# Performance work log

Hardware: AMD Instinct MI355X
Metric: run time of the kernel (lower is better)

The kernel has to match this reference:

```python
import jax, jax.numpy as jnp
import numpy as np
from jax import lax

T = 36          # number of frames (dictionary rows)
MAXITER = 100   # fista maxIter
LAMBD0 = 0.01   # base sparsity weight (scaled by 1/L as in torch code)
TOL = 1e-4      # convergence tolerance


def build_dictionary(Drr, Dtheta, n_frames):
    # Vectorized version of the Python loop over i in range(T).
    i = jnp.arange(n_frames, dtype=Drr.dtype)                     # (T,)
    powr = Drr[None, :] ** i[:, None]                             # (T,N)  Drr^i (Drr>0)
    sign = jnp.where(i[:, None] % 2 == 0, 1.0, -1.0).astype(Drr.dtype)  # (-Drr)^i = (-1)^i Drr^i
    ang = i[:, None] * Dtheta[None, :]
    cosm, sinm = jnp.cos(ang), jnp.sin(ang)
    ones = jnp.ones((n_frames, 1), Drr.dtype)
    dic = jnp.concatenate(
        [ones, powr * cosm, sign * powr * cosm, powr * sinm, sign * powr * sinm],
        axis=1)                                                   # (T, 4N+1)
    G = jnp.linalg.norm(dic, axis=0)                              # column norms
    G = jnp.where(G == 0, jnp.sqrt(jnp.asarray(n_frames, Drr.dtype)), G)
    return dic / G


def softshrink(z, lambd):
    return jnp.sign(z) * jnp.maximum(jnp.abs(z) - lambd, 0.0)


def fista(D, Y):
    # D: (T,K), Y: (B,T,P). torch broadcasts the 2D init state; we carry full (B,K,P).
    DtD = D.T @ D                                                 # (K,K)
    L = jnp.linalg.norm(DtD)      # torch.norm(DtD, 2) = flattened 2-norm (Frobenius)
    linv = 1.0 / L
    DtY = jnp.einsum('tk,btp->bkp', D, Y) * linv                  # (B,K,P)
    K = DtD.shape[0]
    A = jnp.eye(K, dtype=D.dtype) - DtD * linv                    # (K,K)
    lambd = LAMBD0 * linv
    x0 = jnp.zeros_like(DtY)

    def cond(c):
        ii, t, x, y, Ay, done = c
        return (ii < MAXITER) & jnp.logical_not(done)

    def body(c):
        ii, t, x, y, Ay_prev, done = c
        Ay = jnp.einsum('kj,bjp->bkp', A, y)                      # (B,K,P)
        x_new = softshrink(Ay + DtY, lambd)
        t_new = (1.0 + jnp.sqrt(1.0 + 4.0 * t * t)) / 2.0
        tt = (t - 1.0) / t_new
        y_new = (1.0 + tt) * x_new - tt * x
        done = (jnp.linalg.norm((x - x_new).ravel()) / K) < TOL   # device-side convergence test
        return (ii + 1, t_new, x_new, y_new, Ay, done)

    init = (jnp.asarray(0, jnp.int32), jnp.asarray(1.0, D.dtype), x0, x0, x0,
            jnp.asarray(False))
    ii, t, x, y, Ay, done = lax.while_loop(cond, body, init)
    return x, Ay


def setup_inputs() -> dict:
    key = jax.random.key(0)
    k1, k2, k3 = jax.random.split(key, 3)
    N, B, P = 40, 4, 16384
    Drr = (0.8 + 0.2 * jax.random.uniform(k1, (N,))).astype(jnp.float32)   # pole radii near 1
    Dtheta = (np.pi * jax.random.uniform(k2, (N,))).astype(jnp.float32)    # pole angles
    x = jax.random.normal(k3, (B, T, P), dtype=jnp.float32)
    return {"x": x, "Drr": Drr, "Dtheta": Dtheta}


def reference(x, Drr, Dtheta):
    D = build_dictionary(Drr, Dtheta, T)
    sparsecode, _ = fista(D, x)
    return sparsecode
```

## Files before the change

kernel.cpp:

```cpp
#include <hip/hip_runtime.h>
#include <hip/hip_bf16.h>

typedef __attribute__((ext_vector_type(8))) short bf16x8;
typedef __attribute__((ext_vector_type(4))) float f32x4;

#define NITER 100
#define MT 2
#define WS_D     0
#define WS_SCAL  5904
#define WS_A     8192
#define WS_FLOATS (8192 + 192*200)

__device__ __forceinline__ unsigned short f2bf(float x) {
  unsigned u = __builtin_bit_cast(unsigned, x);
  u += 0x7fffu + ((u >> 16) & 1u);
  return (unsigned short)(u >> 16);
}
__device__ __forceinline__ float bf2f(unsigned short h) {
  unsigned u = ((unsigned)h) << 16;
  return __builtin_bit_cast(float, u);
}
__device__ __forceinline__ float ubit(unsigned u) { return __builtin_bit_cast(float, u); }
__device__ __forceinline__ unsigned cvt_pk_bf16(float a, float b) {
  unsigned r;
  asm("v_cvt_pk_bf16_f32 %0, %1, %2" : "=v"(r) : "v"(a), "v"(b));
  return r;
}

__global__ __launch_bounds__(256) void prep_kernel(const float* __restrict__ Drr,
                                                   const float* __restrict__ Dth,
                                                   float* __restrict__ ws)
{
  __shared__ float sD[36 * 164];
  __shared__ float sIG[164];
  __shared__ float sRed[256];
  const int tid = (int)threadIdx.x;

  for (int idx = tid; idx < 36 * 164; idx += 256) {
    int t = idx / 164, k = idx - t * 164;
    float v = 0.0f;
    if (k == 0) v = 1.0f;
    else if (k < 161) {
      int km = k - 1, g = km / 40, n = km - g * 40;
      float pw  = powf(Drr[n], (float)t);
      float ang = (float)t * Dth[n];
      float base = ((g & 2) == 0) ? cosf(ang) : sinf(ang);
      v = pw * base;
      if ((g & 1) && (t & 1)) v = -v;
    }
    sD[idx] = v;
  }
  __syncthreads();
  if (tid < 161) {
    float s = 0.0f;
    for (int t = 0; t < 36; ++t) { float d = sD[t * 164 + tid]; s += d * d; }
    float g = sqrtf(s);
    if (g == 0.0f) g = 6.0f;
    sIG[tid] = 1.0f / g;
  }
  __syncthreads();
  for (int idx = tid; idx < 36 * 164; idx += 256) {
    int k = idx % 164;
    if (k < 161) sD[idx] *= sIG[k];
  }
  __syncthreads();
  {
    float local = 0.0f;
    for (int idx = tid; idx < 36 * 36; idx += 256) {
      int t = idx / 36, t2 = idx - t * 36;
      float dot = 0.0f;
      for (int k = 0; k < 161; ++k) dot += sD[t * 164 + k] * sD[t2 * 164 + k];
      local += dot * dot;
    }
    sRed[tid] = local;
  }
  __syncthreads();
  for (int off = 128; off > 0; off >>= 1) {
    if (tid < off) sRed[tid] += sRed[tid + off];
    __syncthreads();
  }
  const float linv = 1.0f / sqrtf(sRed[0]);

  if (blockIdx.x == 0) {
    for (int idx = tid; idx < 36 * 164; idx += 256) ws[WS_D + idx] = sD[idx];
    if (tid == 0) { ws[WS_SCAL] = linv; ws[WS_SCAL + 1] = 0.01f * linv; }
  }
  const int ENT = (192 * 200 + (int)gridDim.x - 1) / (int)gridDim.x;
  const int base = (int)blockIdx.x * ENT;
  for (int i = tid; i < ENT; i += 256) {
    int e = base + i;
    if (e >= 192 * 200) break;
    int r = e / 200, j = e - r * 200;
    float a = 0.0f;
    if (r < 161 && j < 161) {
      float dot = 0.0f;
      for (int t = 0; t < 36; ++t) dot += sD[t * 164 + r] * sD[t * 164 + j];
      a = ((r == j) ? 1.0f : 0.0f) - dot * linv;
    }
    ws[WS_A + e] = a;
  }
}

union SmemU {
  struct {
    float sD[36 * 164];
    float sIG[164];
    float sRed[512];
  } su;
  unsigned char bounce[2][16 * 384];
};

template <int USE_WS>
__global__ __launch_bounds__(512, 2) void fista_kernel(
    const float* __restrict__ X, const float* __restrict__ Drr,
    const float* __restrict__ Dth, float* __restrict__ out,
    const float* __restrict__ ws)
{
  __shared__ SmemU sm;
  float* sD = sm.su.sD;

  const int tid  = (int)threadIdx.x;
  const int lane = tid & 63;
  const int wv   = tid >> 6;
  const int cl   = lane & 15;
  const int hi   = lane >> 4;
  const int t0   = (wv < 3) ? wv * 2 : 3 + wv;
  const int ntl  = (wv < 3) ? 2 : 1;

  float linv, lambd;
  if constexpr (USE_WS) {
    for (int idx = tid; idx < 36 * 164; idx += 512) sD[idx] = ws[WS_D + idx];
    linv  = ws[WS_SCAL];
    lambd = ws[WS_SCAL + 1];
    __syncthreads();
  } else {
    for (int idx = tid; idx < 36 * 164; idx += 512) {
      int t = idx / 164, k = idx - t * 164;
      float v = 0.0f;
      if (k == 0) v = 1.0f;
      else if (k < 161) {
        int km = k - 1, g = km / 40, n = km - g * 40;
        float pw  = powf(Drr[n], (float)t);
        float ang = (float)t * Dth[n];
        float base = ((g & 2) == 0) ? cosf(ang) : sinf(ang);
        v = pw * base;
        if ((g & 1) && (t & 1)) v = -v;
      }
      sD[idx] = v;
    }
    __syncthreads();
    if (tid < 161) {
      float s = 0.0f;
      for (int t = 0; t < 36; ++t) { float d = sD[t * 164 + tid]; s += d * d; }
      float g = sqrtf(s);
      if (g == 0.0f) g = 6.0f;
      sm.su.sIG[tid] = 1.0f / g;
    }
    __syncthreads();
    for (int idx = tid; idx < 36 * 164; idx += 512) {
      int k = idx % 164;
      if (k < 161) sD[idx] *= sm.su.sIG[k];
    }
    __syncthreads();
    {
      float local = 0.0f;
      for (int idx = tid; idx < 36 * 36; idx += 512) {
        int t = idx / 36, t2 = idx - t * 36;
        float dot = 0.0f;
        for (int k = 0; k < 161; ++k) dot += sD[t * 164 + k] * sD[t2 * 164 + k];
        local += dot * dot;
      }
      sm.su.sRed[tid] = local;
    }
    __syncthreads();
    for (int off = 256; off > 0; off >>= 1) {
      if (tid < off) sm.su.sRed[tid] += sm.su.sRed[tid + off];
      __syncthreads();
    }
    linv  = 1.0f / sqrtf(sm.su.sRed[0]);
    lambd = 0.01f * linv;
  }

  bf16x8 Ah[MT][6], Al[MT][6];
  #pragma unroll
  for (int tau = 0; tau < MT; ++tau) if (tau < ntl) {
    const int r = (t0 + tau) * 16 + cl;
    #pragma unroll
    for (int kt = 0; kt < 6; ++kt) {
      const int k0 = kt * 32 + hi * 8;
      float av[8];
      if constexpr (USE_WS) {
        const float* ap = ws + WS_A + r * 200 + k0;
        f32x4 a0 = *reinterpret_cast<const f32x4*>(ap);
        f32x4 a1 = *reinterpret_cast<const f32x4*>(ap + 4);
        av[0]=a0[0]; av[1]=a0[1]; av[2]=a0[2]; av[3]=a0[3];
        av[4]=a1[0]; av[5]=a1[1]; av[6]=a1[2]; av[7]=a1[3];
      } else {
        float acc8[8];
        #pragma unroll
        for (int j = 0; j < 8; ++j) acc8[j] = 0.0f;
        if (r < 161) {
          for (int t = 0; t < 36; ++t) {
            float vr = sD[t * 164 + r];
            #pragma unroll
            for (int j = 0; j < 8; ++j) acc8[j] += vr * sD[t * 164 + k0 + j];
          }
        }
        #pragma unroll
        for (int j = 0; j < 8; ++j) {
          int k = k0 + j;
          float a = 0.0f;
          if (r < 161 && k < 161) {
            a = -acc8[j] * linv;
            if (r == k) a += 1.0f;
          }
          av[j] = a;
        }
      }
      bf16x8 vh, vl;
      #pragma unroll
      for (int j = 0; j < 8; ++j) {
        unsigned short h = f2bf(av[j]);
        vh[j] = (short)h;
        vl[j] = (short)f2bf(av[j] - bf2f(h));
      }
      Ah[tau][kt] = vh;
      Al[tau][kt] = vl;
    }
  }

  const int c = (int)blockIdx.x * 16 + cl;
  const int b = c >> 14;
  const int p = c & 16383;
  const float* Xc = X + (size_t)b * (36 * 16384) + p;

  f32x4 P0[MT], P1[MT], xe[MT];
  #pragma unroll
  for (int tau = 0; tau < MT; ++tau)
    #pragma unroll
    for (int q = 0; q < 4; ++q) { P0[tau][q] = 0.0f; P1[tau][q] = 0.0f; xe[tau][q] = 0.0f; }

  for (int t = 0; t < 36; ++t) {
    float yv = Xc[(size_t)t * 16384];
    #pragma unroll
    for (int tau = 0; tau < MT; ++tau) if (tau < ntl) {
      const int rt = t0 + tau;
      f32x4 df = *reinterpret_cast<const f32x4*>(sD + t * 164 + rt * 16 + hi * 4);
      #pragma unroll
      for (int q = 0; q < 4; ++q) P0[tau][q] += df[q] * yv;
    }
  }
  #pragma unroll
  for (int tau = 0; tau < MT; ++tau)
    #pragma unroll
    for (int q = 0; q < 4; ++q) {
      int r = (t0 + tau) * 16 + hi * 4 + q;
      P0[tau][q] = (r < 161) ? P0[tau][q] * linv : 0.0f;
    }
  __syncthreads();

  for (int i = tid; i < 2 * 16 * 384 / 16; i += 512) {
    f32x4 z = {0.0f, 0.0f, 0.0f, 0.0f};
    reinterpret_cast<f32x4*>(sm.bounce[0])[i] = z;
  }
  __syncthreads();

  unsigned char* colb = sm.bounce[0] + cl * 384;
  const unsigned swz = (unsigned)((cl & 7) << 4);
  unsigned char* rdA[6];
  #pragma unroll
  for (int kt = 0; kt < 6; ++kt)
    rdA[kt] = colb + (((unsigned)(kt * 64 + hi * 16)) ^ swz);
  unsigned char* wrA[MT];
  #pragma unroll
  for (int tau = 0; tau < MT; ++tau)
    wrA[tau] = colb + (((unsigned)((t0 + tau) * 32 + hi * 8)) ^ swz);

  float tcur = 1.0f, tt = 0.0f;

  auto step = [&](f32x4 (&PC)[MT], f32x4 (&PN)[MT], int boff) {
    const float ttp = tt, c1 = 1.0f + ttp;
    #pragma unroll
    for (int tau = 0; tau < MT; ++tau) if (tau < ntl) {
      float dq_[4];
      #pragma unroll
      for (int q = 0; q < 4; ++q) {
        float u  = c1 * PC[tau][q] - ttp * PN[tau][q];
        float aa = fmaxf(fabsf(u) - lambd, 0.0f);
        float xn = __builtin_copysignf(aa, u);
        dq_[q] = xn - xe[tau][q];
      }
      unsigned w0 = cvt_pk_bf16(dq_[0], dq_[1]);
      unsigned w1 = cvt_pk_bf16(dq_[2], dq_[3]);
      xe[tau][0] += ubit(w0 << 16);
      xe[tau][1] += ubit(w0 & 0xffff0000u);
      xe[tau][2] += ubit(w1 << 16);
      xe[tau][3] += ubit(w1 & 0xffff0000u);
      *reinterpret_cast<uint2*>(wrA[tau] + boff) = make_uint2(w0, w1);
    }
    __syncthreads();
    bf16x8 bh[6];
    #pragma unroll
    for (int kt = 0; kt < 6; ++kt)
      bh[kt] = *reinterpret_cast<const bf16x8*>(rdA[kt] + boff);
    #pragma unroll
    for (int kt = 0; kt < 6; ++kt) {
      #pragma unroll
      for (int tau = 0; tau < MT; ++tau) if (tau < ntl) {
        f32x4 acc = (kt == 0) ? PC[tau] : PN[tau];
        acc = __builtin_amdgcn_mfma_f32_16x16x32_bf16(Ah[tau][kt], bh[kt], acc, 0, 0, 0);
        acc = __builtin_amdgcn_mfma_f32_16x16x32_bf16(Al[tau][kt], bh[kt], acc, 0, 0, 0);
        PN[tau] = acc;
      }
    }
    float tn = 0.5f * (1.0f + sqrtf(1.0f + 4.0f * tcur * tcur));
    tt = (tcur - 1.0f) / tn;
    tcur = tn;
  };

  #pragma unroll 1
  for (int it = 0; it < NITER / 2; ++it) {
    step(P0, P1, 0);
    step(P1, P0, 16 * 384);
  }

  float* op = out + (size_t)b * (161 * 16384) + p;
  #pragma unroll
  for (int tau = 0; tau < MT; ++tau) if (tau < ntl) {
    #pragma unroll
    for (int q = 0; q < 4; ++q) {
      int r = (t0 + tau) * 16 + hi * 4 + q;
      if (r < 161) op[(size_t)r * 16384] = xe[tau][q];
    }
  }
}

extern "C" void kernel_launch(void* const* d_in, const int* in_sizes, int n_in,
                              void* d_out, int out_size, void* d_ws, size_t ws_size,
                              hipStream_t stream) {
  const float* X   = (const float*)d_in[0];
  const float* Drr = (const float*)d_in[1];
  const float* Dth = (const float*)d_in[2];
  float* out = (float*)d_out;
  (void)in_sizes; (void)n_in; (void)out_size;

  if (ws_size >= (size_t)WS_FLOATS * sizeof(float)) {
    float* ws = (float*)d_ws;
    prep_kernel<<<dim3(64), dim3(256), 0, stream>>>(Drr, Dth, ws);
    fista_kernel<1><<<dim3(4096), dim3(512), 0, stream>>>(X, Drr, Dth, out, ws);
  } else {
    fista_kernel<0><<<dim3(4096), dim3(512), 0, stream>>>(X, Drr, Dth, out, nullptr);
  }
}
```

Measured before the change: 1.320 ms.

## Interleave two column groups per block to overlap MFMA with shrink step

Each block now handles two independent 16-column groups, with 6 waves that each own two row tiles. The shrink/update of one group is interleaved with the MFMA matvec of the other through double-buffered LDS bounce buffers, so barrier latency and dependency stalls can be hidden. The FISTA momentum coefficients are precomputed once into LDS instead of being recomputed with sqrt/div every step. A is stored pre-split into bf16 hi/lo in the workspace. The cost is more registers per thread for the duplicated accumulators and more LDS per block, which may reduce occupancy.

```diff
diff --git a/kernel.cpp b/kernel.cpp
--- a/kernel.cpp
+++ b/kernel.cpp
@@ -5,11 +5,10 @@
 typedef __attribute__((ext_vector_type(4))) float f32x4;
 
 #define NITER 100
-#define MT 2
-#define WS_D     0
 #define WS_SCAL  5904
-#define WS_A     8192
-#define WS_FLOATS (8192 + 192*200)
+#define WS_AH    8192
+#define WS_FLOATS (8192 + 19200 + 19200)
+#define BUF1 12288
 
 __device__ __forceinline__ unsigned short f2bf(float x) {
   unsigned u = __builtin_bit_cast(unsigned, x);
@@ -82,9 +81,11 @@
   const float linv = 1.0f / sqrtf(sRed[0]);
 
   if (blockIdx.x == 0) {
-    for (int idx = tid; idx < 36 * 164; idx += 256) ws[WS_D + idx] = sD[idx];
+    for (int idx = tid; idx < 36 * 164; idx += 256) ws[idx] = sD[idx];
     if (tid == 0) { ws[WS_SCAL] = linv; ws[WS_SCAL + 1] = 0.01f * linv; }
   }
+  unsigned short* AH16 = reinterpret_cast<unsigned short*>(ws + WS_AH);
+  unsigned short* AL16 = AH16 + 192 * 200;
   const int ENT = (192 * 200 + (int)gridDim.x - 1) / (int)gridDim.x;
   const int base = (int)blockIdx.x * ENT;
   for (int i = tid; i < ENT; i += 256) {
@@ -97,44 +98,38 @@
       for (int t = 0; t < 36; ++t) dot += sD[t * 164 + r] * sD[t * 164 + j];
       a = ((r == j) ? 1.0f : 0.0f) - dot * linv;
     }
-    ws[WS_A + e] = a;
-  }
-}
-
-union SmemU {
-  struct {
-    float sD[36 * 164];
-    float sIG[164];
-    float sRed[512];
-  } su;
-  unsigned char bounce[2][16 * 384];
-};
+    unsigned short ah = f2bf(a);
+    AH16[e] = ah;
+    AL16[e] = f2bf(a - bf2f(ah));
+  }
+}
 
 template <int USE_WS>
-__global__ __launch_bounds__(512, 2) void fista_kernel(
+__global__ __launch_bounds__(384, 2) void fista_kernel(
     const float* __restrict__ X, const float* __restrict__ Drr,
     const float* __restrict__ Dth, float* __restrict__ out,
     const float* __restrict__ ws)
 {
-  __shared__ SmemU sm;
+  __shared__ union {
+    struct { float sD[36 * 164]; float sIG[164]; float sRed[512]; } su;
+    unsigned char bounce[2][2][16 * 384];
+  } sm;
+  __shared__ float2 sTT[NITER];
+
   float* sD = sm.su.sD;
-
   const int tid  = (int)threadIdx.x;
   const int lane = tid & 63;
   const int wv   = tid >> 6;
   const int cl   = lane & 15;
   const int hi   = lane >> 4;
-  const int t0   = (wv < 3) ? wv * 2 : 3 + wv;
-  const int ntl  = (wv < 3) ? 2 : 1;
 
   float linv, lambd;
   if constexpr (USE_WS) {
-    for (int idx = tid; idx < 36 * 164; idx += 512) sD[idx] = ws[WS_D + idx];
+    for (int idx = tid; idx < 36 * 164; idx += 384) sD[idx] = ws[idx];
     linv  = ws[WS_SCAL];
     lambd = ws[WS_SCAL + 1];
-    __syncthreads();
   } else {
-    for (int idx = tid; idx < 36 * 164; idx += 512) {
+    for (int idx = tid; idx < 36 * 164; idx += 384) {
       int t = idx / 164, k = idx - t * 164;
       float v = 0.0f;
       if (k == 0) v = 1.0f;
@@ -157,20 +152,21 @@
       sm.su.sIG[tid] = 1.0f / g;
     }
     __syncthreads();
-    for (int idx = tid; idx < 36 * 164; idx += 512) {
+    for (int idx = tid; idx < 36 * 164; idx += 384) {
       int k = idx % 164;
       if (k < 161) sD[idx] *= sm.su.sIG[k];
     }
     __syncthreads();
     {
       float local = 0.0f;
-      for (int idx = tid; idx < 36 * 36; idx += 512) {
+      for (int idx = tid; idx < 36 * 36; idx += 384) {
         int t = idx / 36, t2 = idx - t * 36;
         float dot = 0.0f;
         for (int k = 0; k < 161; ++k) dot += sD[t * 164 + k] * sD[t2 * 164 + k];
         local += dot * dot;
       }
       sm.su.sRed[tid] = local;
+      if (tid < 128) sm.su.sRed[384 + tid] = 0.0f;
     }
     __syncthreads();
     for (int off = 256; off > 0; off >>= 1) {
@@ -181,21 +177,36 @@
     lambd = 0.01f * linv;
   }
 
-  bf16x8 Ah[MT][6], Al[MT][6];
-  #pragma unroll
-  for (int tau = 0; tau < MT; ++tau) if (tau < ntl) {
-    const int r = (t0 + tau) * 16 + cl;
-    #pragma unroll
-    for (int kt = 0; kt < 6; ++kt) {
-      const int k0 = kt * 32 + hi * 8;
-      float av[8];
-      if constexpr (USE_WS) {
-        const float* ap = ws + WS_A + r * 200 + k0;
-        f32x4 a0 = *reinterpret_cast<const f32x4*>(ap);
-        f32x4 a1 = *reinterpret_cast<const f32x4*>(ap + 4);
-        av[0]=a0[0]; av[1]=a0[1]; av[2]=a0[2]; av[3]=a0[3];
-        av[4]=a1[0]; av[5]=a1[1]; av[6]=a1[2]; av[7]=a1[3];
-      } else {
+  if (tid == 0) {
+    float t = 1.0f;
+    for (int k = 0; k < NITER; ++k) {
+      float tn = 0.5f * (1.0f + sqrtf(1.0f + 4.0f * t * t));
+      float tt = (t - 1.0f) / tn;
+      sTT[k] = make_float2(tt, 1.0f + tt);
+      t = tn;
+    }
+  }
+
+  bf16x8 Ah[2][6], Al[2][6];
+  if constexpr (USE_WS) {
+    const unsigned short* AH16 = reinterpret_cast<const unsigned short*>(ws + WS_AH);
+    const unsigned short* AL16 = AH16 + 192 * 200;
+    #pragma unroll
+    for (int tau = 0; tau < 2; ++tau) {
+      const int r = (2 * wv + tau) * 16 + cl;
+      #pragma unroll
+      for (int kt = 0; kt < 6; ++kt) {
+        Ah[tau][kt] = *reinterpret_cast<const bf16x8*>(AH16 + r * 200 + kt * 32 + hi * 8);
+        Al[tau][kt] = *reinterpret_cast<const bf16x8*>(AL16 + r * 200 + kt * 32 + hi * 8);
+      }
+    }
+  } else {
+    #pragma unroll
+    for (int tau = 0; tau < 2; ++tau) {
+      const int r = (2 * wv + tau) * 16 + cl;
+      #pragma unroll
+      for (int kt = 0; kt < 6; ++kt) {
+        const int k0 = kt * 32 + hi * 8;
         float acc8[8];
         #pragma unroll
         for (int j = 0; j < 8; ++j) acc8[j] = 0.0f;
@@ -206,6 +217,7 @@
             for (int j = 0; j < 8; ++j) acc8[j] += vr * sD[t * 164 + k0 + j];
           }
         }
+        bf16x8 vh, vl;
         #pragma unroll
         for (int j = 0; j < 8; ++j) {
           int k = k0 + j;
@@ -214,74 +226,72 @@
             a = -acc8[j] * linv;
             if (r == k) a += 1.0f;
           }
-          av[j] = a;
+          unsigned short h = f2bf(a);
+          vh[j] = (short)h;
+          vl[j] = (short)f2bf(a - bf2f(h));
         }
-      }
-      bf16x8 vh, vl;
-      #pragma unroll
-      for (int j = 0; j < 8; ++j) {
-        unsigned short h = f2bf(av[j]);
-        vh[j] = (short)h;
-        vl[j] = (short)f2bf(av[j] - bf2f(h));
-      }
-      Ah[tau][kt] = vh;
-      Al[tau][kt] = vl;
-    }
-  }
-
-  const int c = (int)blockIdx.x * 16 + cl;
-  const int b = c >> 14;
-  const int p = c & 16383;
-  const float* Xc = X + (size_t)b * (36 * 16384) + p;
-
-  f32x4 P0[MT], P1[MT], xe[MT];
+        Ah[tau][kt] = vh;
+        Al[tau][kt] = vl;
+      }
+    }
+  }
+
+  const int cb = (int)blockIdx.x * 32;
+  const int cA = cb + cl, cB = cb + 16 + cl;
+  const float* XA = X + (size_t)(cA >> 14) * (36 * 16384) + (cA & 16383);
+  const float* XB = X + (size_t)(cB >> 14) * (36 * 16384) + (cB & 16383);
+
+  f32x4 Pa0[2], Pb0[2], xe0[2], Pa1[2], Pb1[2], xe1[2];
   #pragma unroll
-  for (int tau = 0; tau < MT; ++tau)
-    #pragma unroll
-    for (int q = 0; q < 4; ++q) { P0[tau][q] = 0.0f; P1[tau][q] = 0.0f; xe[tau][q] = 0.0f; }
+  for (int tau = 0; tau < 2; ++tau)
+    #pragma unroll
+    for (int q = 0; q < 4; ++q) {
+      Pa0[tau][q] = 0.0f; Pb0[tau][q] = 0.0f; xe0[tau][q] = 0.0f;
+      Pa1[tau][q] = 0.0f; Pb1[tau][q] = 0.0f; xe1[tau][q] = 0.0f;
+    }
 
   for (int t = 0; t < 36; ++t) {
-    float yv = Xc[(size_t)t * 16384];
-    #pragma unroll
-    for (int tau = 0; tau < MT; ++tau) if (tau < ntl) {
-      const int rt = t0 + tau;
-      f32x4 df = *reinterpret_cast<const f32x4*>(sD + t * 164 + rt * 16 + hi * 4);
-      #pragma unroll
-      for (int q = 0; q < 4; ++q) P0[tau][q] += df[q] * yv;
+    float yA = XA[(size_t)t * 16384];
+    float yB = XB[(size_t)t * 16384];
+    #pragma unroll
+    for (int tau = 0; tau < 2; ++tau) {
+      f32x4 df = *reinterpret_cast<const f32x4*>(sD + t * 164 + (2 * wv + tau) * 16 + hi * 4);
+      #pragma unroll
+      for (int q = 0; q < 4; ++q) { Pa0[tau][q] += df[q] * yA; Pa1[tau][q] += df[q] * yB; }
     }
   }
   #pragma unroll
-  for (int tau = 0; tau < MT; ++tau)
+  for (int tau = 0; tau < 2; ++tau)
     #pragma unroll
     for (int q = 0; q < 4; ++q) {
-      int r = (t0 + tau) * 16 + hi * 4 + q;
-      P0[tau][q] = (r < 161) ? P0[tau][q] * linv : 0.0f;
-    }
-  __syncthreads();
-
-  for (int i = tid; i < 2 * 16 * 384 / 16; i += 512) {
-    f32x4 z = {0.0f, 0.0f, 0.0f, 0.0f};
-    reinterpret_cast<f32x4*>(sm.bounce[0])[i] = z;
-  }
-  __syncthreads();
-
-  unsigned char* colb = sm.bounce[0] + cl * 384;
+      int r = (2 * wv + tau) * 16 + hi * 4 + q;
+      Pa0[tau][q] = (r < 161) ? Pa0[tau][q] * linv : 0.0f;
+      Pa1[tau][q] = (r < 161) ? Pa1[tau][q] * linv : 0.0f;
+    }
+  __syncthreads();
+
+  unsigned char* colb0 = &sm.bounce[0][0][0] + cl * 384;
+  unsigned char* colb1 = &sm.bounce[0][1][0] + cl * 384;
   const unsigned swz = (unsigned)((cl & 7) << 4);
-  unsigned char* rdA[6];
+  unsigned char* pe0 = colb0 + ((unsigned)(hi * 16) ^ swz);
+  unsigned char* po0 = colb0 + ((unsigned)(64 + hi * 16) ^ swz);
+  unsigned char* pe1 = colb1 + ((unsigned)(hi * 16) ^ swz);
+  unsigned char* po1 = colb1 + ((unsigned)(64 + hi * 16) ^ swz);
+  unsigned char* wr0[2];
+  unsigned char* wr1[2];
   #pragma unroll
-  for (int kt = 0; kt < 6; ++kt)
-    rdA[kt] = colb + (((unsigned)(kt * 64 + hi * 16)) ^ swz);
-  unsigned char* wrA[MT];
-  #pragma unroll
-  for (int tau = 0; tau < MT; ++tau)
-    wrA[tau] = colb + (((unsigned)((t0 + tau) * 32 + hi * 8)) ^ swz);
-
-  float tcur = 1.0f, tt = 0.0f;
-
-  auto step = [&](f32x4 (&PC)[MT], f32x4 (&PN)[MT], int boff) {
-    const float ttp = tt, c1 = 1.0f + ttp;
-    #pragma unroll
-    for (int tau = 0; tau < MT; ++tau) if (tau < ntl) {
+  for (int tau = 0; tau < 2; ++tau) {
+    unsigned off = ((unsigned)((2 * wv + tau) * 32 + hi * 8)) ^ swz;
+    wr0[tau] = colb0 + off;
+    wr1[tau] = colb1 + off;
+  }
+
+  auto sh = [&](f32x4 (&PC)[2], f32x4 (&PN)[2], f32x4 (&xe)[2], int it,
+                unsigned char* (&wr)[2], int boff) {
+    float2 tt2 = sTT[it];
+    const float ttp = tt2.x, c1 = tt2.y;
+    #pragma unroll
+    for (int tau = 0; tau < 2; ++tau) {
       float dq_[4];
       #pragma unroll
       for (int q = 0; q < 4; ++q) {
@@ -296,43 +306,57 @@
       xe[tau][1] += ubit(w0 & 0xffff0000u);
       xe[tau][2] += ubit(w1 << 16);
       xe[tau][3] += ubit(w1 & 0xffff0000u);
-      *reinterpret_cast<uint2*>(wrA[tau] + boff) = make_uint2(w0, w1);
-    }
-    __syncthreads();
+      *reinterpret_cast<uint2*>(wr[tau] + boff) = make_uint2(w0, w1);
+    }
+  };
+  auto mf = [&](f32x4 (&PC)[2], f32x4 (&PN)[2],
+                const unsigned char* pe, const unsigned char* po, int boff) {
     bf16x8 bh[6];
-    #pragma unroll
-    for (int kt = 0; kt < 6; ++kt)
-      bh[kt] = *reinterpret_cast<const bf16x8*>(rdA[kt] + boff);
-    #pragma unroll
-    for (int kt = 0; kt < 6; ++kt) {
-      #pragma unroll
-      for (int tau = 0; tau < MT; ++tau) if (tau < ntl) {
-        f32x4 acc = (kt == 0) ? PC[tau] : PN[tau];
+    bh[0] = *reinterpret_cast<const bf16x8*>(pe + boff + 0);
+    bh[1] = *reinterpret_cast<const bf16x8*>(po + boff + 0);
+    bh[2] = *reinterpret_cast<const bf16x8*>(pe + boff + 128);
+    bh[3] = *reinterpret_cast<const bf16x8*>(po + boff + 128);
+    bh[4] = *reinterpret_cast<const bf16x8*>(pe + boff + 256);
+    bh[5] = *reinterpret_cast<const bf16x8*>(po + boff + 256);
+    #pragma unroll
+    for (int tau = 0; tau < 2; ++tau) {
+      f32x4 acc = PC[tau];
+      #pragma unroll
+      for (int kt = 0; kt < 6; ++kt) {
         acc = __builtin_amdgcn_mfma_f32_16x16x32_bf16(Ah[tau][kt], bh[kt], acc, 0, 0, 0);
         acc = __builtin_amdgcn_mfma_f32_16x16x32_bf16(Al[tau][kt], bh[kt], acc, 0, 0, 0);
-        PN[tau] = acc;
-      }
-    }
-    float tn = 0.5f * (1.0f + sqrtf(1.0f + 4.0f * tcur * tcur));
-    tt = (tcur - 1.0f) / tn;
-    tcur = tn;
+      }
+      PN[tau] = acc;
+    }
   };
 
+  sh(Pa0, Pb0, xe0, 0, wr0, 0);
   #pragma unroll 1
-  for (int it = 0; it < NITER / 2; ++it) {
-    step(P0, P1, 0);
-    step(P1, P0, 16 * 384);
-  }
-
-  float* op = out + (size_t)b * (161 * 16384) + p;
+  for (int j = 0; j < NITER / 2; ++j) {
+    const int it = 2 * j;
+    __syncthreads();
+    mf(Pa0, Pb0, pe0, po0, 0);     sh(Pa1, Pb1, xe1, it, wr1, 0);
+    __syncthreads();
+    mf(Pa1, Pb1, pe1, po1, 0);     sh(Pb0, Pa0, xe0, it + 1, wr0, BUF1);
+    __syncthreads();
+    mf(Pb0, Pa0, pe0, po0, BUF1);  sh(Pb1, Pa1, xe1, it + 1, wr1, BUF1);
+    __syncthreads();
+    mf(Pb1, Pa1, pe1, po1, BUF1);
+    if (j < NITER / 2 - 1) sh(Pa0, Pb0, xe0, it + 2, wr0, 0);
+  }
+
+  float* oA = out + (size_t)(cA >> 14) * (161 * 16384) + (cA & 16383);
+  float* oB = out + (size_t)(cB >> 14) * (161 * 16384) + (cB & 16383);
   #pragma unroll
-  for (int tau = 0; tau < MT; ++tau) if (tau < ntl) {
+  for (int tau = 0; tau < 2; ++tau)
     #pragma unroll
     for (int q = 0; q < 4; ++q) {
-      int r = (t0 + tau) * 16 + hi * 4 + q;
-      if (r < 161) op[(size_t)r * 16384] = xe[tau][q];
-    }
-  }
+      int r = (2 * wv + tau) * 16 + hi * 4 + q;
+      if (r < 161) {
+        oA[(size_t)r * 16384] = xe0[tau][q];
+        oB[(size_t)r * 16384] = xe1[tau][q];
+      }
+    }
 }
 
 extern "C" void kernel_launch(void* const* d_in, const int* in_sizes, int n_in,
@@ -347,8 +371,8 @@
   if (ws_size >= (size_t)WS_FLOATS * sizeof(float)) {
     float* ws = (float*)d_ws;
     prep_kernel<<<dim3(64), dim3(256), 0, stream>>>(Drr, Dth, ws);
-    fista_kernel<1><<<dim3(4096), dim3(512), 0, stream>>>(X, Drr, Dth, out, ws);
+    fista_kernel<1><<<dim3(2048), dim3(384), 0, stream>>>(X, Drr, Dth, out, ws);
   } else {
-    fista_kernel<0><<<dim3(4096), dim3(512), 0, stream>>>(X, Drr, Dth, out, nullptr);
-  }
-}
+    fista_kernel<0><<<dim3(2048), dim3(384), 0, stream>>>(X, Drr, Dth, out, nullptr);
+  }
+}
```

After: 1.532 ms. 1.16x slower.

## Give each wave one row tile with 768-thread blocks and precompute FISTA constants

Applied to the files above, without the earlier changes.

Raises the block from 8 to 12 waves so each wave owns exactly one 16-row tile of the iteration matrix, instead of some waves holding two. This removes the load imbalance where two-tile waves set the per-step critical path before each barrier. The prep kernel now also stores A already split into bf16 hi/lo parts, plus a table of momentum coefficients that the main loop reads from LDS instead of recomputing sqrt and divide each step. The trade-off: a 12th wave computes an all-padding tile, and launch bounds of 768 threads at 3 blocks per CU squeeze registers per thread, which risks spills.

```diff
diff --git a/kernel.cpp b/kernel.cpp
--- a/kernel.cpp
+++ b/kernel.cpp
@@ -5,11 +5,11 @@
 typedef __attribute__((ext_vector_type(4))) float f32x4;
 
 #define NITER 100
-#define MT 2
-#define WS_D     0
 #define WS_SCAL  5904
-#define WS_A     8192
-#define WS_FLOATS (8192 + 192*200)
+#define WS_TT    6016
+#define WS_AH    8192
+#define WS_FLOATS (8192 + 19200 + 19200)
+#define BUFB 6144
 
 __device__ __forceinline__ unsigned short f2bf(float x) {
   unsigned u = __builtin_bit_cast(unsigned, x);
@@ -82,9 +82,22 @@
   const float linv = 1.0f / sqrtf(sRed[0]);
 
   if (blockIdx.x == 0) {
-    for (int idx = tid; idx < 36 * 164; idx += 256) ws[WS_D + idx] = sD[idx];
-    if (tid == 0) { ws[WS_SCAL] = linv; ws[WS_SCAL + 1] = 0.01f * linv; }
-  }
+    for (int idx = tid; idx < 36 * 164; idx += 256) ws[idx] = sD[idx];
+    if (tid == 0) {
+      ws[WS_SCAL] = linv;
+      ws[WS_SCAL + 1] = 0.01f * linv;
+      float t = 1.0f;
+      for (int k = 0; k < NITER; ++k) {
+        float tn = 0.5f * (1.0f + sqrtf(1.0f + 4.0f * t * t));
+        float tt = (t - 1.0f) / tn;
+        ws[WS_TT + 2 * k]     = tt;
+        ws[WS_TT + 2 * k + 1] = 1.0f + tt;
+        t = tn;
+      }
+    }
+  }
+  unsigned short* AH16 = reinterpret_cast<unsigned short*>(ws + WS_AH);
+  unsigned short* AL16 = AH16 + 192 * 200;
   const int ENT = (192 * 200 + (int)gridDim.x - 1) / (int)gridDim.x;
   const int base = (int)blockIdx.x * ENT;
   for (int i = tid; i < ENT; i += 256) {
@@ -97,26 +110,22 @@
       for (int t = 0; t < 36; ++t) dot += sD[t * 164 + r] * sD[t * 164 + j];
       a = ((r == j) ? 1.0f : 0.0f) - dot * linv;
     }
-    ws[WS_A + e] = a;
-  }
-}
-
-union SmemU {
-  struct {
-    float sD[36 * 164];
-    float sIG[164];
-    float sRed[512];
-  } su;
-  unsigned char bounce[2][16 * 384];
-};
+    unsigned short ah = f2bf(a);
+    AH16[e] = ah;
+    AL16[e] = f2bf(a - bf2f(ah));
+  }
+}
 
 template <int USE_WS>
-__global__ __launch_bounds__(512, 2) void fista_kernel(
+__global__ __launch_bounds__(768, 3) void fista_kernel(
     const float* __restrict__ X, const float* __restrict__ Drr,
     const float* __restrict__ Dth, float* __restrict__ out,
     const float* __restrict__ ws)
 {
-  __shared__ SmemU sm;
+  __shared__ union {
+    struct { float sD[36 * 164]; float sIG[164]; float sRed[768]; } su;
+    struct { unsigned char bounce[2][BUFB]; float2 tt[128]; } lp;
+  } sm;
   float* sD = sm.su.sD;
 
   const int tid  = (int)threadIdx.x;
@@ -124,17 +133,15 @@
   const int wv   = tid >> 6;
   const int cl   = lane & 15;
   const int hi   = lane >> 4;
-  const int t0   = (wv < 3) ? wv * 2 : 3 + wv;
-  const int ntl  = (wv < 3) ? 2 : 1;
 
   float linv, lambd;
   if constexpr (USE_WS) {
-    for (int idx = tid; idx < 36 * 164; idx += 512) sD[idx] = ws[WS_D + idx];
+    for (int idx = tid; idx < 36 * 164; idx += 768) sD[idx] = ws[idx];
     linv  = ws[WS_SCAL];
     lambd = ws[WS_SCAL + 1];
     __syncthreads();
   } else {
-    for (int idx = tid; idx < 36 * 164; idx += 512) {
+    for (int idx = tid; idx < 36 * 164; idx += 768) {
       int t = idx / 164, k = idx - t * 164;
       float v = 0.0f;
       if (k == 0) v = 1.0f;
@@ -157,14 +164,14 @@
       sm.su.sIG[tid] = 1.0f / g;
     }
     __syncthreads();
-    for (int idx = tid; idx < 36 * 164; idx += 512) {
+    for (int idx = tid; idx < 36 * 164; idx += 768) {
       int k = idx % 164;
       if (k < 161) sD[idx] *= sm.su.sIG[k];
     }
     __syncthreads();
     {
       float local = 0.0f;
-      for (int idx = tid; idx < 36 * 36; idx += 512) {
+      for (int idx = tid; idx < 36 * 36; idx += 768) {
         int t = idx / 36, t2 = idx - t * 36;
         float dot = 0.0f;
         for (int k = 0; k < 161; ++k) dot += sD[t * 164 + k] * sD[t2 * 164 + k];
@@ -173,7 +180,9 @@
       sm.su.sRed[tid] = local;
     }
     __syncthreads();
-    for (int off = 256; off > 0; off >>= 1) {
+    if (tid < 256) sm.su.sRed[tid] += sm.su.sRed[tid + 256] + sm.su.sRed[tid + 512];
+    __syncthreads();
+    for (int off = 128; off > 0; off >>= 1) {
       if (tid < off) sm.su.sRed[tid] += sm.su.sRed[tid + off];
       __syncthreads();
     }
@@ -181,51 +190,46 @@
     lambd = 0.01f * linv;
   }
 
-  bf16x8 Ah[MT][6], Al[MT][6];
-  #pragma unroll
-  for (int tau = 0; tau < MT; ++tau) if (tau < ntl) {
-    const int r = (t0 + tau) * 16 + cl;
+  bf16x8 Ah[6], Al[6];
+  if constexpr (USE_WS) {
+    const unsigned short* AH16 = reinterpret_cast<const unsigned short*>(ws + WS_AH);
+    const unsigned short* AL16 = AH16 + 192 * 200;
+    const int r = wv * 16 + cl;
+    #pragma unroll
+    for (int kt = 0; kt < 6; ++kt) {
+      Ah[kt] = *reinterpret_cast<const bf16x8*>(AH16 + r * 200 + kt * 32 + hi * 8);
+      Al[kt] = *reinterpret_cast<const bf16x8*>(AL16 + r * 200 + kt * 32 + hi * 8);
+    }
+  } else {
+    const int r = wv * 16 + cl;
     #pragma unroll
     for (int kt = 0; kt < 6; ++kt) {
       const int k0 = kt * 32 + hi * 8;
-      float av[8];
-      if constexpr (USE_WS) {
-        const float* ap = ws + WS_A + r * 200 + k0;
-        f32x4 a0 = *reinterpret_cast<const f32x4*>(ap);
-        f32x4 a1 = *reinterpret_cast<const f32x4*>(ap + 4);
-        av[0]=a0[0]; av[1]=a0[1]; av[2]=a0[2]; av[3]=a0[3];
-        av[4]=a1[0]; av[5]=a1[1]; av[6]=a1[2]; av[7]=a1[3];
-      } else {
-        float acc8[8];
-        #pragma unroll
-        for (int j = 0; j < 8; ++j) acc8[j] = 0.0f;
-        if (r < 161) {
-          for (int t = 0; t < 36; ++t) {
-            float vr = sD[t * 164 + r];
-            #pragma unroll
-            for (int j = 0; j < 8; ++j) acc8[j] += vr * sD[t * 164 + k0 + j];
-          }
-        }
-        #pragma unroll
-        for (int j = 0; j < 8; ++j) {
-          int k = k0 + j;
-          float a = 0.0f;
-          if (r < 161 && k < 161) {
-            a = -acc8[j] * linv;
-            if (r == k) a += 1.0f;
-          }
-          av[j] = a;
+      float acc8[8];
+      #pragma unroll
+      for (int j = 0; j < 8; ++j) acc8[j] = 0.0f;
+      if (r < 161) {
+        for (int t = 0; t < 36; ++t) {
+          float vr = sD[t * 164 + r];
+          #pragma unroll
+          for (int j = 0; j < 8; ++j) acc8[j] += vr * sD[t * 164 + k0 + j];
         }
       }
       bf16x8 vh, vl;
       #pragma unroll
       for (int j = 0; j < 8; ++j) {
-        unsigned short h = f2bf(av[j]);
+        int k = k0 + j;
+        float a = 0.0f;
+        if (r < 161 && k < 161) {
+          a = -acc8[j] * linv;
+          if (r == k) a += 1.0f;
+        }
+        unsigned short h = f2bf(a);
         vh[j] = (short)h;
-        vl[j] = (short)f2bf(av[j] - bf2f(h));
-      }
-      Ah[tau][kt] = vh;
-      Al[tau][kt] = vl;
+        vl[j] = (short)f2bf(a - bf2f(h));
+      }
+      Ah[kt] = vh;
+      Al[kt] = vl;
     }
   }
 
@@ -234,104 +238,90 @@
   const int p = c & 16383;
   const float* Xc = X + (size_t)b * (36 * 16384) + p;
 
-  f32x4 P0[MT], P1[MT], xe[MT];
+  f32x4 P0, P1, xe;
   #pragma unroll
-  for (int tau = 0; tau < MT; ++tau)
-    #pragma unroll
-    for (int q = 0; q < 4; ++q) { P0[tau][q] = 0.0f; P1[tau][q] = 0.0f; xe[tau][q] = 0.0f; }
+  for (int q = 0; q < 4; ++q) { P0[q] = 0.0f; P1[q] = 0.0f; xe[q] = 0.0f; }
 
   for (int t = 0; t < 36; ++t) {
     float yv = Xc[(size_t)t * 16384];
-    #pragma unroll
-    for (int tau = 0; tau < MT; ++tau) if (tau < ntl) {
-      const int rt = t0 + tau;
-      f32x4 df = *reinterpret_cast<const f32x4*>(sD + t * 164 + rt * 16 + hi * 4);
-      #pragma unroll
-      for (int q = 0; q < 4; ++q) P0[tau][q] += df[q] * yv;
-    }
+    f32x4 df = *reinterpret_cast<const f32x4*>(sD + t * 164 + wv * 16 + hi * 4);
+    #pragma unroll
+    for (int q = 0; q < 4; ++q) P0[q] += df[q] * yv;
   }
   #pragma unroll
-  for (int tau = 0; tau < MT; ++tau)
-    #pragma unroll
-    for (int q = 0; q < 4; ++q) {
-      int r = (t0 + tau) * 16 + hi * 4 + q;
-      P0[tau][q] = (r < 161) ? P0[tau][q] * linv : 0.0f;
-    }
-  __syncthreads();
-
-  for (int i = tid; i < 2 * 16 * 384 / 16; i += 512) {
-    f32x4 z = {0.0f, 0.0f, 0.0f, 0.0f};
-    reinterpret_cast<f32x4*>(sm.bounce[0])[i] = z;
-  }
-  __syncthreads();
-
-  unsigned char* colb = sm.bounce[0] + cl * 384;
+  for (int q = 0; q < 4; ++q) {
+    int r = wv * 16 + hi * 4 + q;
+    P0[q] = (r < 161) ? P0[q] * linv : 0.0f;
+  }
+  __syncthreads();
+
+  if constexpr (USE_WS) {
+    const float2* wt = reinterpret_cast<const float2*>(ws + WS_TT);
+    for (int i = tid; i < NITER; i += 768) sm.lp.tt[i] = wt[i];
+  } else {
+    if (tid == 0) {
+      float t = 1.0f;
+      for (int k = 0; k < NITER; ++k) {
+        float tn = 0.5f * (1.0f + sqrtf(1.0f + 4.0f * t * t));
+        float tt = (t - 1.0f) / tn;
+        sm.lp.tt[k] = make_float2(tt, 1.0f + tt);
+        t = tn;
+      }
+    }
+  }
+  __syncthreads();
+
+  unsigned char* colb = &sm.lp.bounce[0][0] + cl * 384;
   const unsigned swz = (unsigned)((cl & 7) << 4);
   unsigned char* rdA[6];
   #pragma unroll
   for (int kt = 0; kt < 6; ++kt)
     rdA[kt] = colb + (((unsigned)(kt * 64 + hi * 16)) ^ swz);
-  unsigned char* wrA[MT];
-  #pragma unroll
-  for (int tau = 0; tau < MT; ++tau)
-    wrA[tau] = colb + (((unsigned)((t0 + tau) * 32 + hi * 8)) ^ swz);
-
-  float tcur = 1.0f, tt = 0.0f;
-
-  auto step = [&](f32x4 (&PC)[MT], f32x4 (&PN)[MT], int boff) {
-    const float ttp = tt, c1 = 1.0f + ttp;
-    #pragma unroll
-    for (int tau = 0; tau < MT; ++tau) if (tau < ntl) {
-      float dq_[4];
-      #pragma unroll
-      for (int q = 0; q < 4; ++q) {
-        float u  = c1 * PC[tau][q] - ttp * PN[tau][q];
-        float aa = fmaxf(fabsf(u) - lambd, 0.0f);
-        float xn = __builtin_copysignf(aa, u);
-        dq_[q] = xn - xe[tau][q];
-      }
-      unsigned w0 = cvt_pk_bf16(dq_[0], dq_[1]);
-      unsigned w1 = cvt_pk_bf16(dq_[2], dq_[3]);
-      xe[tau][0] += ubit(w0 << 16);
-      xe[tau][1] += ubit(w0 & 0xffff0000u);
-      xe[tau][2] += ubit(w1 << 16);
-      xe[tau][3] += ubit(w1 & 0xffff0000u);
-      *reinterpret_cast<uint2*>(wrA[tau] + boff) = make_uint2(w0, w1);
-    }
+  unsigned char* wrA = colb + (((unsigned)(wv * 32 + hi * 8)) ^ swz);
+
+  auto step = [&](f32x4& PC, f32x4& PN, int it, int boff) {
+    float2 t2 = sm.lp.tt[it];
+    const float ttp = t2.x, c1 = t2.y;
+    float dq_[4];
+    #pragma unroll
+    for (int q = 0; q < 4; ++q) {
+      float u  = c1 * PC[q] - ttp * PN[q];
+      float aa = fmaxf(fabsf(u) - lambd, 0.0f);
+      float xn = __builtin_copysignf(aa, u);
+      dq_[q] = xn - xe[q];
+    }
+    unsigned w0 = cvt_pk_bf16(dq_[0], dq_[1]);
+    unsigned w1 = cvt_pk_bf16(dq_[2], dq_[3]);
+    xe[0] += ubit(w0 << 16);
+    xe[1] += ubit(w0 & 0xffff0000u);
+    xe[2] += ubit(w1 << 16);
+    xe[3] += ubit(w1 & 0xffff0000u);
+    *reinterpret_cast<uint2*>(wrA + boff) = make_uint2(w0, w1);
     __syncthreads();
     bf16x8 bh[6];
     #pragma unroll
     for (int kt = 0; kt < 6; ++kt)
       bh[kt] = *reinterpret_cast<const bf16x8*>(rdA[kt] + boff);
+    f32x4 acc = PC;
     #pragma unroll
     for (int kt = 0; kt < 6; ++kt) {
-      #pragma unroll
-      for (int tau = 0; tau < MT; ++tau) if (tau < ntl) {
-        f32x4 acc = (kt == 0) ? PC[tau] : PN[tau];
-        acc = __builtin_amdgcn_mfma_f32_16x16x32_bf16(Ah[tau][kt], bh[kt], acc, 0, 0, 0);
-        acc = __builtin_amdgcn_mfma_f32_16x16x32_bf16(Al[tau][kt], bh[kt], acc, 0, 0, 0);
-        PN[tau] = acc;
-      }
-    }
-    float tn = 0.5f * (1.0f + sqrtf(1.0f + 4.0f * tcur * tcur));
-    tt = (tcur - 1.0f) / tn;
-    tcur = tn;
+      acc = __builtin_amdgcn_mfma_f32_16x16x32_bf16(Ah[kt], bh[kt], acc, 0, 0, 0);
+      acc = __builtin_amdgcn_mfma_f32_16x16x32_bf16(Al[kt], bh[kt], acc, 0, 0, 0);
+    }
+    PN = acc;
   };
 
   #pragma unroll 1
-  for (int it = 0; it < NITER / 2; ++it) {
-    step(P0, P1, 0);
-    step(P1, P0, 16 * 384);
+  for (int j = 0; j < NITER / 2; ++j) {
+    step(P0, P1, 2 * j, 0);
+    step(P1, P0, 2 * j + 1, BUFB);
   }
 
   float* op = out + (size_t)b * (161 * 16384) + p;
   #pragma unroll
-  for (int tau = 0; tau < MT; ++tau) if (tau < ntl) {
-    #pragma unroll
-    for (int q = 0; q < 4; ++q) {
-      int r = (t0 + tau) * 16 + hi * 4 + q;
-      if (r < 161) op[(size_t)r * 16384] = xe[tau][q];
-    }
+  for (int q = 0; q < 4; ++q) {
+    int r = wv * 16 + hi * 4 + q;
+    if (r < 161) op[(size_t)r * 16384] = xe[q];
   }
 }
 
@@ -347,8 +337,8 @@
   if (ws_size >= (size_t)WS_FLOATS * sizeof(float)) {
     float* ws = (float*)d_ws;
     prep_kernel<<<dim3(64), dim3(256), 0, stream>>>(Drr, Dth, ws);
-    fista_kernel<1><<<dim3(4096), dim3(512), 0, stream>>>(X, Drr, Dth, out, ws);
+    fista_kernel<1><<<dim3(4096), dim3(768), 0, stream>>>(X, Drr, Dth, out, ws);
   } else {
-    fista_kernel<0><<<dim3(4096), dim3(512), 0, stream>>>(X, Drr, Dth, out, nullptr);
-  }
-}
+    fista_kernel<0><<<dim3(4096), dim3(768), 0, stream>>>(X, Drr, Dth, out, nullptr);
+  }
+}
```

Result: no change. 1.341 ms (+1.5%).
